# Kernel tuning notes

Measured on AMD Instinct MI355X. Metric: run time of the kernel, lower is better.

The kernel has to match this reference:

```python
import jax, jax.numpy as jnp
import numpy as np


def _fft2c(x, axes):
    # fftshift(fft2(ifftshift(x), norm='ortho'))
    return jnp.fft.fftshift(
        jnp.fft.fft2(jnp.fft.ifftshift(x, axes=axes), axes=axes, norm='ortho'),
        axes=axes)


def _warp(img, flow):
    # img: [Nx,Ny] complex, flow: [Nx,Ny,2] (displacements along x,y)
    # Dense equivalent of the sparse bilinear motion matrix apply.
    Nx, Ny = img.shape
    gx = jnp.arange(Nx, dtype=flow.dtype)[:, None]
    gy = jnp.arange(Ny, dtype=flow.dtype)[None, :]
    x = jnp.clip(gx + flow[:, :, 0], 0.0, Nx - 1)
    y = jnp.clip(gy + flow[:, :, 1], 0.0, Ny - 1)
    x0 = jnp.clip(jnp.floor(x), 0, Nx - 2).astype(jnp.int32)
    y0 = jnp.clip(jnp.floor(y), 0, Ny - 2).astype(jnp.int32)
    wx = x - x0
    wy = y - y0
    x1 = x0 + 1
    y1 = y0 + 1
    v00 = img[x0, y0]
    v01 = img[x0, y1]
    v10 = img[x1, y0]
    v11 = img[x1, y1]
    return ((1 - wx) * (1 - wy)) * v00 + ((1 - wx) * wy) * v01 \
         + (wx * (1 - wy)) * v10 + (wx * wy) * v11


def setup_inputs() -> dict:
    key = jax.random.key(0)
    k = jax.random.split(key, 6)
    Nx, Ny, Nc, Nt = 256, 256, 16, 24
    return {
        'image_real': jax.random.normal(k[0], (Nx, Ny), dtype=jnp.float32),
        'image_imag': jax.random.normal(k[1], (Nx, Ny), dtype=jnp.float32),
        'mask': jax.random.uniform(k[2], (Nx, Ny, Nc, Nt), dtype=jnp.float32),
        'smaps_real': jax.random.normal(k[3], (Nx, Ny, Nc), dtype=jnp.float32),
        'smaps_imag': jax.random.normal(k[4], (Nx, Ny, Nc), dtype=jnp.float32),
        'flow': jax.random.normal(k[5], (Nx, Ny, 2, Nt), dtype=jnp.float32) * 2.0,
    }


def reference(image_real, image_imag, mask, smaps_real, smaps_imag, flow):
    img = image_real + 1j * image_imag            # [Nx,Ny]
    smaps = smaps_real + 1j * smaps_imag          # [Nx,Ny,Nc]
    flow_t = jnp.moveaxis(flow, -1, 0)            # [Nt,Nx,Ny,2]
    warped = jax.vmap(_warp, in_axes=(None, 0))(img, flow_t)   # [Nt,Nx,Ny]
    coil = warped[:, :, :, None] * smaps[None]    # [Nt,Nx,Ny,Nc]
    k = _fft2c(coil, axes=(1, 2))                 # [Nt,Nx,Ny,Nc]
    mask_t = jnp.moveaxis(mask, -1, 0)            # [Nt,Nx,Ny,Nc]
    out = jnp.sum(k * mask_t, axis=0)             # [Nx,Ny,Nc] complex
    # stack real/imag for a real-valued output (complex not in dtype enum)
    return jnp.stack([out.real, out.imag], axis=0)  # [2,Nx,Ny,Nc]
```

## Files before the change

kernel.cpp:

```cpp
#include <hip/hip_runtime.h>
#include <math.h>

#define NCD 16
#define NTD 24
#define NPIX 65536

struct c32 { float x, y; };

__device__ __forceinline__ c32 cadd(c32 a, c32 b){ return {a.x+b.x, a.y+b.y}; }
__device__ __forceinline__ c32 csub(c32 a, c32 b){ return {a.x-b.x, a.y-b.y}; }
__device__ __forceinline__ c32 cmul(c32 a, c32 b){ return {a.x*b.x - a.y*b.y, a.x*b.y + a.y*b.x}; }
__device__ __forceinline__ c32 cnegi(c32 a){ return {a.y, -a.x}; }

__device__ __forceinline__ unsigned short f2h(float f) {
  return __builtin_bit_cast(unsigned short, (_Float16)f);
}
__device__ __forceinline__ float h2f(unsigned short s) {
  return (float)__builtin_bit_cast(_Float16, s);
}
__device__ __forceinline__ unsigned int pk2(c32 v) {
  return (unsigned int)f2h(v.x) | ((unsigned int)f2h(v.y) << 16);
}
__device__ __forceinline__ c32 up2(unsigned int u) {
  c32 r; r.x = h2f((unsigned short)(u & 0xffffu)); r.y = h2f((unsigned short)(u >> 16));
  return r;
}

__constant__ float W16R_[16] = {
  1.0f, 0.9238795325f, 0.7071067812f, 0.3826834324f,
  0.0f,-0.3826834324f,-0.7071067812f,-0.9238795325f,
 -1.0f,-0.9238795325f,-0.7071067812f,-0.3826834324f,
  0.0f, 0.3826834324f, 0.7071067812f, 0.9238795325f };
__constant__ float W16I_[16] = {
  0.0f,-0.3826834324f,-0.7071067812f,-0.9238795325f,
 -1.0f,-0.9238795325f,-0.7071067812f,-0.3826834324f,
  0.0f, 0.3826834324f, 0.7071067812f, 0.9238795325f,
  1.0f, 0.9238795325f, 0.7071067812f, 0.3826834324f };

__device__ __forceinline__ int revmap(int p) { return ((p & 3) << 2) | (p >> 2); }

__device__ __forceinline__ void dft16(c32 v[16]) {
  c32 y[16];
#pragma unroll
  for (int j = 0; j < 4; ++j) {
    c32 a = v[j], b = v[j+4], c = v[j+8], d = v[j+12];
    c32 t0 = cadd(a,c), t1 = csub(a,c), t2 = cadd(b,d), t3 = cnegi(csub(b,d));
    y[j] = cadd(t0,t2);
    if (j == 0) {
      y[4]  = cadd(t1,t3);
      y[8]  = csub(t0,t2);
      y[12] = csub(t1,t3);
    } else {
      c32 w1 = {W16R_[j],        W16I_[j]};
      c32 w2 = {W16R_[(2*j)&15], W16I_[(2*j)&15]};
      c32 w3 = {W16R_[(3*j)&15], W16I_[(3*j)&15]};
      y[4+j]  = cmul(cadd(t1,t3), w1);
      y[8+j]  = cmul(csub(t0,t2), w2);
      y[12+j] = cmul(csub(t1,t3), w3);
    }
  }
#pragma unroll
  for (int q = 0; q < 4; ++q) {
    c32 a = y[4*q], b = y[4*q+1], c = y[4*q+2], d = y[4*q+3];
    c32 t0 = cadd(a,c), t1 = csub(a,c), t2 = cadd(b,d), t3 = cnegi(csub(b,d));
    v[4*q+0] = cadd(t0,t2);
    v[4*q+1] = cadd(t1,t3);
    v[4*q+2] = csub(t0,t2);
    v[4*q+3] = csub(t1,t3);
  }
}

__device__ __forceinline__ void fft256(c32 v[16], const unsigned int twh[16],
                                       c32* lds, int g, int lane) {
  dft16(v);
#pragma unroll
  for (int p = 0; p < 16; ++p) v[p] = cmul(v[p], up2(twh[p]));
  __syncthreads();
#pragma unroll
  for (int p = 0; p < 16; ++p) {
    int k1 = revmap(p);
    lds[g*256 + k1*16 + (lane ^ k1)] = v[p];
  }
  __syncthreads();
#pragma unroll
  for (int j = 0; j < 16; ++j)
    v[j] = lds[g*256 + lane*16 + (j ^ lane)];
  dft16(v);
}

__device__ __forceinline__ void fft256h(c32 v[16], const unsigned int twh[16],
                                        unsigned int* ldsu, int g, int lane) {
  dft16(v);
#pragma unroll
  for (int p = 0; p < 16; ++p) v[p] = cmul(v[p], up2(twh[p]));
  __syncthreads();
#pragma unroll
  for (int p = 0; p < 16; ++p) {
    int k1 = revmap(p);
    ldsu[g*272 + k1*17 + lane] = pk2(v[p]);
  }
  __syncthreads();
#pragma unroll
  for (int j = 0; j < 16; ++j)
    v[j] = up2(ldsu[g*272 + lane*17 + j]);
  dft16(v);
}

__global__ __launch_bounds__(256) void kS(const float* __restrict__ sre,
                                          const float* __restrict__ sim,
                                          unsigned int* __restrict__ smapsTh) {
  __shared__ float lre[16*260];
  __shared__ float lim[16*260];
  int nx = blockIdx.x, tid = threadIdx.x;
#pragma unroll
  for (int it = 0; it < 16; ++it) {
    int e = it*256 + tid;
    int ny = e >> 4, c = e & 15;
    lre[c*260 + ny] = sre[(size_t)nx*4096 + e];
    lim[c*260 + ny] = sim[(size_t)nx*4096 + e];
  }
  __syncthreads();
#pragma unroll
  for (int c = 0; c < 16; ++c) {
    c32 v = { lre[c*260 + tid], lim[c*260 + tid] };
    smapsTh[(size_t)c*NPIX + nx*256 + tid] = pk2(v);
  }
}

__global__ __launch_bounds__(256) void kW(const float* __restrict__ ire,
                                          const float* __restrict__ iim,
                                          const float* __restrict__ flow,
                                          unsigned int* __restrict__ wh) {
  __shared__ float fl[256*49];
  int nx = blockIdx.x, tid = threadIdx.x;
  const float* src = flow + (size_t)nx*12288;
#pragma unroll
  for (int it = 0; it < 48; ++it) {
    int e = it*256 + tid;
    fl[(e/48)*49 + (e%48)] = src[e];
  }
  __syncthreads();
  int ny = tid;
  float s = ((nx + ny) & 1) ? -1.0f : 1.0f;
  for (int t = 0; t < NTD; ++t) {
    float fx = fl[ny*49 + t];
    float fy = fl[ny*49 + 24 + t];
    float xf = fminf(fmaxf((float)nx + fx, 0.0f), 255.0f);
    float yf = fminf(fmaxf((float)ny + fy, 0.0f), 255.0f);
    float x0f = fminf(floorf(xf), 254.0f);
    float y0f = fminf(floorf(yf), 254.0f);
    int i00 = (int)x0f * 256 + (int)y0f;
    float wx = xf - x0f, wy = yf - y0f;
    float w00 = (1.f-wx)*(1.f-wy), w01 = (1.f-wx)*wy;
    float w10 = wx*(1.f-wy),       w11 = wx*wy;
    float re = w00*ire[i00] + w01*ire[i00+1] + w10*ire[i00+256] + w11*ire[i00+257];
    float im = w00*iim[i00] + w01*iim[i00+1] + w10*iim[i00+256] + w11*iim[i00+257];
    c32 v = { re*s, im*s };
    wh[(size_t)t*NPIX + nx*256 + ny] = pk2(v);
  }
}

__global__ __launch_bounds__(256) void kM(const float* __restrict__ mask,
                                          unsigned int* __restrict__ maskTh,
                                          int t0, int chunkT) {
  __shared__ unsigned short lm[256*49];
  int ky = blockIdx.x, c0 = blockIdx.y*2, tid = threadIdx.x;
  int nct = 2*chunkT;
  int total = 256*nct;
  for (int e = tid; e < total; e += 256) {
    int kx = e / nct, ctl = e - kx*nct;
    int hi = (ctl >= chunkT) ? 1 : 0;
    int cc = c0 + hi;
    int tt = t0 + ctl - hi*chunkT;
    lm[kx*49 + ctl] = f2h(mask[(size_t)kx*98304 + ky*384 + cc*24 + tt]);
  }
  __syncthreads();
  int wtotal = nct*128;
  for (int e = tid; e < wtotal; e += 256) {
    int ctl = e >> 7;
    int posh = (e & 127) * 2;
    int hi = (ctl >= chunkT) ? 1 : 0;
    int cc = c0 + hi;
    int ltt = ctl - hi*chunkT;
    int kxa = ((posh & 15) << 4) | (posh >> 4);
    int kxb = (((posh+1) & 15) << 4) | ((posh+1) >> 4);
    unsigned int a = lm[kxa*49 + ctl], b = lm[kxb*49 + ctl];
    size_t base = (((((size_t)ltt*256 + ky)*16 + cc) << 8) + posh) >> 1;
    maskTh[base] = a | (b << 16);
  }
}

__global__ __launch_bounds__(256) void kA(const unsigned int* __restrict__ wh,
                                          const unsigned int* __restrict__ smapsTh,
                                          unsigned int* __restrict__ Y1h, int t0) {
  __shared__ unsigned int fftws[4352];
  __shared__ unsigned int stage[4096];
  int tid = threadIdx.x, g = tid >> 4, lane = tid & 15;
  int lt = blockIdx.y, t = t0 + lt;
  int nx0 = blockIdx.x*16, nx = nx0 + g;
  int c0 = blockIdx.z*4;

  unsigned int wr[16];
  const unsigned int* wrow = wh + (size_t)t*NPIX + nx*256;
#pragma unroll
  for (int n1 = 0; n1 < 16; ++n1) wr[n1] = wrow[n1*16 + lane];

  unsigned int twh[16];
#pragma unroll
  for (int p = 0; p < 16; ++p) {
    int k1 = revmap(p);
    float ang = -6.283185307179586f * (float)(lane * k1) * (1.0f/256.0f);
    float sv, cv; __sincosf(ang, &sv, &cv);
    c32 tw; tw.x = cv; tw.y = sv;
    twh[p] = pk2(tw);
  }

  unsigned int su[16];
  {
    const unsigned int* srow = smapsTh + (size_t)c0*NPIX + nx*256;
#pragma unroll
    for (int n1 = 0; n1 < 16; ++n1) su[n1] = srow[n1*16 + lane];
  }

  for (int ci = 0; ci < 4; ++ci) {
    int c = c0 + ci;
    c32 v[16];
#pragma unroll
    for (int n1 = 0; n1 < 16; ++n1) v[n1] = cmul(up2(wr[n1]), up2(su[n1]));
    if (ci < 3) {
      const unsigned int* srow = smapsTh + (size_t)(c + 1)*NPIX + nx*256;
#pragma unroll
      for (int n1 = 0; n1 < 16; ++n1) su[n1] = srow[n1*16 + lane];
    }
    fft256h(v, twh, fftws, g, lane);
#pragma unroll
    for (int p = 0; p < 16; ++p) {
      int ky = lane + 16*revmap(p);
      stage[ky*16 + (g ^ lane)] = pk2(v[p]);
    }
    __syncthreads();
    unsigned int* dst = Y1h + (((size_t)lt*16 + c) << 16) + nx0;
#pragma unroll
    for (int it = 0; it < 16; ++it) {
      int e = it*256 + tid;
      int ky = e >> 4, j = e & 15;
      dst[(size_t)ky*256 + j] = stage[ky*16 + (j ^ (ky & 15))];
    }
  }
}

__global__ __launch_bounds__(256) void kB(const unsigned int* __restrict__ Y1h,
                                          const unsigned int* __restrict__ maskTh,
                                          float* __restrict__ out,
                                          int chunkT, int accum) {
  __shared__ c32 lds[4096];
  int tid = threadIdx.x, g = tid >> 4, lane = tid & 15;
  int ci = g & 3, tp = g >> 2;
  int cq = blockIdx.x, ky = blockIdx.y;
  int c = cq*4 + ci;

  unsigned int twh[16];
#pragma unroll
  for (int p = 0; p < 16; ++p) {
    int k1 = revmap(p);
    float ang = -6.283185307179586f * (float)(lane * k1) * (1.0f/256.0f);
    float sv, cv; __sincosf(ang, &sv, &cv);
    c32 tw; tw.x = cv; tw.y = sv;
    twh[p] = pk2(tw);
  }

  c32 acc[16];
#pragma unroll
  for (int p = 0; p < 16; ++p) { acc[p].x = 0.f; acc[p].y = 0.f; }
  float wsc = (((lane + ky) & 1) ? -1.0f : 1.0f) * (1.0f/256.0f);

  int iters = (chunkT + 3) >> 2;
  unsigned int u[16];
#pragma unroll
  for (int n1 = 0; n1 < 16; ++n1) u[n1] = 0;
  if (tp < chunkT) {
    const unsigned int* row = Y1h + ((size_t)(tp*16 + c)*256 + ky)*256;
#pragma unroll
    for (int n1 = 0; n1 < 16; ++n1) u[n1] = row[n1*16 + lane];
  }

  for (int ii = 0; ii < iters; ++ii) {
    int lt = tp + 4*ii;
    bool act = lt < chunkT;
    int lts = act ? lt : 0;
    const unsigned int* mp = maskTh
        + (((((size_t)lts*256 + ky)*16 + c) << 8) >> 1) + lane*8;
    unsigned int mu[8];
#pragma unroll
    for (int q = 0; q < 8; ++q) mu[q] = mp[q];
    c32 v[16];
#pragma unroll
    for (int n1 = 0; n1 < 16; ++n1) v[n1] = up2(u[n1]);
    int ltn = tp + 4*(ii+1);
    if (ltn < chunkT) {
      const unsigned int* row = Y1h + ((size_t)(ltn*16 + c)*256 + ky)*256;
#pragma unroll
      for (int n1 = 0; n1 < 16; ++n1) u[n1] = row[n1*16 + lane];
    }
    fft256(v, twh, lds, g, lane);
    if (act) {
#pragma unroll
      for (int p = 0; p < 16; ++p) {
        int j = revmap(p);
        unsigned int um = mu[j >> 1];
        unsigned short us = (j & 1) ? (unsigned short)(um >> 16)
                                    : (unsigned short)(um & 0xffffu);
        float m = h2f(us) * wsc;
        acc[p].x += v[p].x * m;
        acc[p].y += v[p].y * m;
      }
    }
  }
  __syncthreads();
#pragma unroll
  for (int p = 0; p < 16; ++p) lds[g*256 + p*16 + lane] = acc[p];
  __syncthreads();
  int kx = tid;
  int lane2 = kx & 15, pp = revmap(kx >> 4);
  float vre[4], vim[4];
#pragma unroll
  for (int c2 = 0; c2 < 4; ++c2) {
    float sx = 0.f, sy = 0.f;
#pragma unroll
    for (int t2 = 0; t2 < 4; ++t2) {
      c32 a = lds[(t2*4 + c2)*256 + pp*16 + lane2];
      sx += a.x; sy += a.y;
    }
    vre[c2] = sx; vim[c2] = sy;
  }
  size_t o = (((size_t)kx << 8) + ky)*16 + cq*4;
  float4* pre = (float4*)(out + o);
  float4* pim = (float4*)(out + (size_t)NPIX*NCD + o);
  float4 R = {vre[0], vre[1], vre[2], vre[3]};
  float4 I = {vim[0], vim[1], vim[2], vim[3]};
  if (accum) {
    float4 r0 = *pre, i0 = *pim;
    R.x += r0.x; R.y += r0.y; R.z += r0.z; R.w += r0.w;
    I.x += i0.x; I.y += i0.y; I.z += i0.z; I.w += i0.w;
  }
  *pre = R; *pim = I;
}

extern "C" void kernel_launch(void* const* d_in, const int* in_sizes, int n_in,
                              void* d_out, int out_size, void* d_ws, size_t ws_size,
                              hipStream_t stream) {
  const float* ire  = (const float*)d_in[0];
  const float* iim  = (const float*)d_in[1];
  const float* mask = (const float*)d_in[2];
  const float* sre  = (const float*)d_in[3];
  const float* sim  = (const float*)d_in[4];
  const float* flow = (const float*)d_in[5];
  float* out = (float*)d_out;

  char* ws = (char*)d_ws;
  const size_t smapsT_b = (size_t)NCD * NPIX * 4;
  const size_t w_b      = (size_t)NTD * NPIX * 4;
  unsigned int* smapsTh = (unsigned int*)ws;
  unsigned int* whbuf   = (unsigned int*)(ws + smapsT_b);
  size_t base = smapsT_b + w_b;
  size_t rem  = (ws_size > base) ? ws_size - base : 0;

  const size_t maskT_per_t = (size_t)NPIX * NCD * 2;
  const size_t y1_per_t    = (size_t)NCD * NPIX * 4;
  int chunk = 1;
  const int cands[8] = {24, 12, 8, 6, 4, 3, 2, 1};
  for (int i = 0; i < 8; ++i) {
    if ((size_t)cands[i] * (maskT_per_t + y1_per_t) <= rem) { chunk = cands[i]; break; }
  }
  unsigned int* maskTh = (unsigned int*)(ws + base);
  unsigned int* Y1h    = (unsigned int*)(ws + base + (size_t)chunk * maskT_per_t);

  kS<<<256, 256, 0, stream>>>(sre, sim, smapsTh);
  kW<<<256, 256, 0, stream>>>(ire, iim, flow, whbuf);
  for (int t0 = 0; t0 < NTD; t0 += chunk) {
    kM<<<dim3(256, 8), 256, 0, stream>>>(mask, maskTh, t0, chunk);
    kA<<<dim3(16, chunk, 4), 256, 0, stream>>>(whbuf, smapsTh, Y1h, t0);
    kB<<<dim3(4, 256), 256, 0, stream>>>(Y1h, maskTh, out, chunk, t0 > 0 ? 1 : 0);
  }
}
```

Baseline: 286.5 us.

## Merge smaps, warp and mask preprocessing into one launch when fully chunked

Adds a combined preprocessing kernel kP whose block index picks one of three jobs: mask transpose to fp16, smaps packing, or the flow-based warp. When the workspace fits all 24 frames, this replaces three separate launches (kS, kW, kM). The three jobs then run concurrently on the GPU and two launch overheads are dropped. The mask and flow loads also switch to float4 vector reads, and shared memory per block shrinks, which may let more blocks share a CU. The old multi-launch path stays as a fallback for smaller workspaces.

```diff
diff --git a/kernel.cpp b/kernel.cpp
--- a/kernel.cpp
+++ b/kernel.cpp
@@ -106,6 +106,115 @@
   dft16(v);
 }
 
+__device__ __forceinline__ void warp_one(const float* __restrict__ ire,
+                                         const float* __restrict__ iim,
+                                         int nx, int ny, float fx, float fy,
+                                         float s, c32* v) {
+  float xf = fminf(fmaxf((float)nx + fx, 0.0f), 255.0f);
+  float yf = fminf(fmaxf((float)ny + fy, 0.0f), 255.0f);
+  float x0f = fminf(floorf(xf), 254.0f);
+  float y0f = fminf(floorf(yf), 254.0f);
+  int i00 = (int)x0f * 256 + (int)y0f;
+  float wx = xf - x0f, wy = yf - y0f;
+  float w00 = (1.f-wx)*(1.f-wy), w01 = (1.f-wx)*wy;
+  float w10 = wx*(1.f-wy),       w11 = wx*wy;
+  float re = w00*ire[i00] + w01*ire[i00+1] + w10*ire[i00+256] + w11*ire[i00+257];
+  float im = w00*iim[i00] + w01*iim[i00+1] + w10*iim[i00+256] + w11*iim[i00+257];
+  v->x = re*s; v->y = im*s;
+}
+
+__global__ __launch_bounds__(256) void kP(const float* __restrict__ sre,
+                                          const float* __restrict__ sim,
+                                          const float* __restrict__ ire,
+                                          const float* __restrict__ iim,
+                                          const float* __restrict__ flow,
+                                          const float* __restrict__ mask,
+                                          unsigned int* __restrict__ smapsTh,
+                                          unsigned int* __restrict__ wh,
+                                          unsigned int* __restrict__ maskTh) {
+  __shared__ float shf[6400];
+  int bx = blockIdx.x, tid = threadIdx.x;
+  if (bx < 2048) {
+    unsigned short* lm = (unsigned short*)shf;
+    int ky = bx >> 3, c0 = (bx & 7) * 2;
+    const float4* m4 = (const float4*)mask;
+    size_t rowbase = ((size_t)ky*384 + (size_t)c0*24) >> 2;
+#pragma unroll
+    for (int i = 0; i < 12; ++i) {
+      int idx = tid + 256*i;
+      int kx = idx / 12, r = idx - kx*12;
+      float4 v = m4[(size_t)kx*24576 + rowbase + r];
+      int b = kx*49 + r*4;
+      lm[b+0] = f2h(v.x); lm[b+1] = f2h(v.y);
+      lm[b+2] = f2h(v.z); lm[b+3] = f2h(v.w);
+    }
+    __syncthreads();
+#pragma unroll
+    for (int i = 0; i < 24; ++i) {
+      int e = tid + 256*i;
+      int ctl = e >> 7;
+      int posh = (e & 127) * 2;
+      int hi = (ctl >= 24) ? 1 : 0;
+      int cc = c0 + hi;
+      int ltt = ctl - hi*24;
+      int kxa = ((posh & 15) << 4) | (posh >> 4);
+      int kxb = kxa + 16;
+      unsigned int a = lm[kxa*49 + ctl], b = lm[kxb*49 + ctl];
+      size_t base = (((((size_t)ltt*256 + ky)*16 + cc) << 8) + posh) >> 1;
+      maskTh[base] = a | (b << 16);
+    }
+  } else if (bx < 2304) {
+    int nx = bx - 2048;
+    float rre[16];
+#pragma unroll
+    for (int it = 0; it < 16; ++it) {
+      int e = it*256 + tid;
+      shf[(e & 15)*260 + (e >> 4)] = sre[(size_t)nx*4096 + e];
+    }
+    __syncthreads();
+#pragma unroll
+    for (int c = 0; c < 16; ++c) rre[c] = shf[c*260 + tid];
+    __syncthreads();
+#pragma unroll
+    for (int it = 0; it < 16; ++it) {
+      int e = it*256 + tid;
+      shf[(e & 15)*260 + (e >> 4)] = sim[(size_t)nx*4096 + e];
+    }
+    __syncthreads();
+#pragma unroll
+    for (int c = 0; c < 16; ++c) {
+      c32 v = { rre[c], shf[c*260 + tid] };
+      smapsTh[(size_t)c*NPIX + nx*256 + tid] = pk2(v);
+    }
+  } else {
+    int nx = bx - 2304;
+    int ny = tid;
+    float s = ((nx + ny) & 1) ? -1.0f : 1.0f;
+    const float4* f4 = (const float4*)(flow + (size_t)nx*12288);
+    for (int h = 0; h < 2; ++h) {
+      if (h) __syncthreads();
+#pragma unroll
+      for (int i = 0; i < 6; ++i) {
+        int idx = tid + 256*i;
+        int yy = idx / 6, q = idx - yy*6;
+        int d = q / 3, r = q - d*3;
+        float4 v = f4[(yy*48 + d*24 + h*12) / 4 + r];
+        int b = yy*25 + d*12 + r*4;
+        shf[b+0] = v.x; shf[b+1] = v.y; shf[b+2] = v.z; shf[b+3] = v.w;
+      }
+      __syncthreads();
+      for (int tl = 0; tl < 12; ++tl) {
+        int t = h*12 + tl;
+        float fx = shf[ny*25 + tl];
+        float fy = shf[ny*25 + 12 + tl];
+        c32 v;
+        warp_one(ire, iim, nx, ny, fx, fy, s, &v);
+        wh[(size_t)t*NPIX + nx*256 + ny] = pk2(v);
+      }
+    }
+  }
+}
+
 __global__ __launch_bounds__(256) void kS(const float* __restrict__ sre,
                                           const float* __restrict__ sim,
                                           unsigned int* __restrict__ smapsTh) {
@@ -115,9 +224,8 @@
 #pragma unroll
   for (int it = 0; it < 16; ++it) {
     int e = it*256 + tid;
-    int ny = e >> 4, c = e & 15;
-    lre[c*260 + ny] = sre[(size_t)nx*4096 + e];
-    lim[c*260 + ny] = sim[(size_t)nx*4096 + e];
+    lre[(e & 15)*260 + (e >> 4)] = sre[(size_t)nx*4096 + e];
+    lim[(e & 15)*260 + (e >> 4)] = sim[(size_t)nx*4096 + e];
   }
   __syncthreads();
 #pragma unroll
@@ -143,19 +251,8 @@
   int ny = tid;
   float s = ((nx + ny) & 1) ? -1.0f : 1.0f;
   for (int t = 0; t < NTD; ++t) {
-    float fx = fl[ny*49 + t];
-    float fy = fl[ny*49 + 24 + t];
-    float xf = fminf(fmaxf((float)nx + fx, 0.0f), 255.0f);
-    float yf = fminf(fmaxf((float)ny + fy, 0.0f), 255.0f);
-    float x0f = fminf(floorf(xf), 254.0f);
-    float y0f = fminf(floorf(yf), 254.0f);
-    int i00 = (int)x0f * 256 + (int)y0f;
-    float wx = xf - x0f, wy = yf - y0f;
-    float w00 = (1.f-wx)*(1.f-wy), w01 = (1.f-wx)*wy;
-    float w10 = wx*(1.f-wy),       w11 = wx*wy;
-    float re = w00*ire[i00] + w01*ire[i00+1] + w10*ire[i00+256] + w11*ire[i00+257];
-    float im = w00*iim[i00] + w01*iim[i00+1] + w10*iim[i00+256] + w11*iim[i00+257];
-    c32 v = { re*s, im*s };
+    c32 v;
+    warp_one(ire, iim, nx, ny, fl[ny*49 + t], fl[ny*49 + 24 + t], s, &v);
     wh[(size_t)t*NPIX + nx*256 + ny] = pk2(v);
   }
 }
@@ -183,7 +280,7 @@
     int cc = c0 + hi;
     int ltt = ctl - hi*chunkT;
     int kxa = ((posh & 15) << 4) | (posh >> 4);
-    int kxb = (((posh+1) & 15) << 4) | ((posh+1) >> 4);
+    int kxb = kxa + 16;
     unsigned int a = lm[kxa*49 + ctl], b = lm[kxb*49 + ctl];
     size_t base = (((((size_t)ltt*256 + ky)*16 + cc) << 8) + posh) >> 1;
     maskTh[base] = a | (b << 16);
@@ -375,11 +472,18 @@
   unsigned int* maskTh = (unsigned int*)(ws + base);
   unsigned int* Y1h    = (unsigned int*)(ws + base + (size_t)chunk * maskT_per_t);
 
-  kS<<<256, 256, 0, stream>>>(sre, sim, smapsTh);
-  kW<<<256, 256, 0, stream>>>(ire, iim, flow, whbuf);
-  for (int t0 = 0; t0 < NTD; t0 += chunk) {
-    kM<<<dim3(256, 8), 256, 0, stream>>>(mask, maskTh, t0, chunk);
-    kA<<<dim3(16, chunk, 4), 256, 0, stream>>>(whbuf, smapsTh, Y1h, t0);
-    kB<<<dim3(4, 256), 256, 0, stream>>>(Y1h, maskTh, out, chunk, t0 > 0 ? 1 : 0);
-  }
-}
+  if (chunk == 24) {
+    kP<<<2560, 256, 0, stream>>>(sre, sim, ire, iim, flow, mask,
+                                 smapsTh, whbuf, maskTh);
+    kA<<<dim3(16, 24, 4), 256, 0, stream>>>(whbuf, smapsTh, Y1h, 0);
+    kB<<<dim3(4, 256), 256, 0, stream>>>(Y1h, maskTh, out, 24, 0);
+  } else {
+    kS<<<256, 256, 0, stream>>>(sre, sim, smapsTh);
+    kW<<<256, 256, 0, stream>>>(ire, iim, flow, whbuf);
+    for (int t0 = 0; t0 < NTD; t0 += chunk) {
+      kM<<<dim3(256, 8), 256, 0, stream>>>(mask, maskTh, t0, chunk);
+      kA<<<dim3(16, chunk, 4), 256, 0, stream>>>(whbuf, smapsTh, Y1h, t0);
+      kB<<<dim3(4, 256), 256, 0, stream>>>(Y1h, maskTh, out, chunk, t0 > 0 ? 1 : 0);
+    }
+  }
+}
```

Result: faster. 279.7 us (-2.4%).
